# Optimization experiments

Measured on AMD Instinct MI355X. Metric: run time of the kernel, lower is better.

## Reference

```python
import jax, jax.numpy as jnp
import numpy as np

B, T, D = 2, 2048, 1024
H = 16
HD = D // H
SCALE = 1.0 / np.sqrt(HD).astype(np.float32)


def setup_inputs() -> dict:
    key = jax.random.key(0)
    ks = jax.random.split(key, 5)
    std = 1.0 / np.sqrt(D).astype(np.float32)
    x = jax.random.normal(ks[0], (B, T, D), dtype=jnp.float32)
    Wqkvt = jax.random.normal(ks[1], (D, 4 * D), dtype=jnp.float32) * std
    bqkvt = jax.random.normal(ks[2], (4 * D,), dtype=jnp.float32) * 0.02
    Wout = jax.random.normal(ks[3], (D, D), dtype=jnp.float32) * std
    bout = jax.random.normal(ks[4], (D,), dtype=jnp.float32) * 0.02
    return {"x": x, "Wqkvt": Wqkvt, "bqkvt": bqkvt, "Wout": Wout, "bout": bout}


def reference(x, Wqkvt, bqkvt, Wout, bout):
    b, t, d = x.shape
    # fused qkvt projection -> [B,T,4,H,HD]
    qkvt = (x @ Wqkvt + bqkvt).reshape(b, t, 4, H, HD)
    # -> [B,H,T,HD] each
    q, k, v, tt = [jnp.transpose(qkvt[:, :, i], (0, 2, 1, 3)) for i in range(4)]

    # standard dot-product scores [B,H,T,T]
    scores_dot = jnp.einsum('bhqd,bhkd->bhqk', q, k)
    # triplet term: (q*t) against cumsum over keys of (k*v)/sqrt(hd)
    kv = k * v * SCALE
    kv_cum = jnp.cumsum(kv, axis=2)  # causal prefix over key positions
    scores_trip = jnp.einsum('bhqd,bhkd->bhqk', q * tt, kv_cum)

    scores = (scores_dot + scores_trip) * SCALE
    causal = jnp.triu(jnp.ones((t, t), dtype=bool), k=1)
    scores = jnp.where(causal[None, None], -jnp.inf, scores)

    attn = jax.nn.softmax(scores, axis=-1)
    out = jnp.einsum('bhqk,bhkd->bhqd', attn, v)  # [B,H,T,HD]
    out = jnp.transpose(out, (0, 2, 1, 3)).reshape(b, t, d)
    return out @ Wout + bout
```

## Files before the change

kernel.cpp:

```cpp
#include <hip/hip_runtime.h>

#define T_SEQ 2048
#define D_MODEL 1024
#define NH 16
#define HD 64
#define BH_TOT 32
#define M_ROWS 4096
#define NT 32
#define SCALE 0.125f
#define BHT (BH_TOT * T_SEQ)
#define LOG2E 1.44269504f
#define TAU 2.885f

typedef _Float16 h8 __attribute__((ext_vector_type(8)));
typedef _Float16 h4 __attribute__((ext_vector_type(4)));
typedef float f32x4 __attribute__((ext_vector_type(4)));

__device__ __forceinline__ f32x4 mfma_h(h8 a, h8 b, f32x4 c) {
    return __builtin_amdgcn_mfma_f32_16x16x32_f16(a, b, c, 0, 0, 0);
}

__device__ __forceinline__ void gload16(const _Float16* g, _Float16* l) {
    __builtin_amdgcn_global_load_lds(
        (const __attribute__((address_space(1))) unsigned int*)g,
        (__attribute__((address_space(3))) unsigned int*)l, 16, 0, 0);
}

__global__ void k_convert(const float* __restrict__ in, _Float16* __restrict__ out, int n) {
    int i = (blockIdx.x * blockDim.x + threadIdx.x) * 4;
    if (i < n) {
        float4 v = *(const float4*)(in + i);
        h4 o;
        o[0] = (_Float16)v.x; o[1] = (_Float16)v.y;
        o[2] = (_Float16)v.z; o[3] = (_Float16)v.w;
        *(h4*)(out + i) = o;
    }
}

__global__ void k_transpose(const float* __restrict__ in, _Float16* __restrict__ out, int K, int N) {
    __shared__ float tile[32][33];
    int nb = blockIdx.x * 32, kb = blockIdx.y * 32;
    int tx = threadIdx.x & 31, ty = threadIdx.x >> 5;
    #pragma unroll
    for (int i = 0; i < 32; i += 8)
        tile[ty + i][tx] = in[(size_t)(kb + ty + i) * N + (nb + tx)];
    __syncthreads();
    #pragma unroll
    for (int i = 0; i < 32; i += 8)
        out[(size_t)(nb + ty + i) * K + (kb + tx)] = (_Float16)tile[tx][ty + i];
}

template<int MODE>
__launch_bounds__(256, 2)
__global__ void k_gemm(const _Float16* __restrict__ A, const _Float16* __restrict__ Bt,
                       int M, int N, int K, const float* __restrict__ bias,
                       _Float16* __restrict__ qo, _Float16* __restrict__ kho,
                       _Float16* __restrict__ kfo, _Float16* __restrict__ vo,
                       _Float16* __restrict__ vfo, _Float16* __restrict__ to,
                       float* __restrict__ cOut)
{
    __shared__ __align__(16) _Float16 lA[2][128 * 64];
    __shared__ __align__(16) _Float16 lB[2][128 * 64];
    const int tid = threadIdx.x;
    const int wid = tid >> 6, lane = tid & 63, lrow = lane & 15, lg = lane >> 4;
    const int wm = wid >> 1, wn = wid & 1;
    const int m0 = blockIdx.x * 128, n0 = blockIdx.y * 128;

    f32x4 acc[4][4];
    #pragma unroll
    for (int i = 0; i < 4; i++)
        #pragma unroll
        for (int j = 0; j < 4; j++) acc[i][j] = (f32x4){0.f, 0.f, 0.f, 0.f};

    const int rin = lane >> 3, gcol = lane & 7;
    const int scol = (gcol ^ rin) * 8;
    const _Float16* gA = A + (size_t)(m0 + 32 * wid + rin) * K + scol;
    const _Float16* gB = Bt + (size_t)(n0 + 32 * wid + rin) * K + scol;

    const int r7 = lrow & 7;
    const int nk = K >> 6;

    #pragma unroll
    for (int i = 0; i < 4; i++) {
        gload16(gA + (size_t)(8 * i) * K, &lA[0][32 * wid * 64 + 8 * i * 64]);
        gload16(gB + (size_t)(8 * i) * K, &lB[0][32 * wid * 64 + 8 * i * 64]);
    }
    __syncthreads();

    for (int kt = 0; kt < nk; ++kt) {
        const int cur = kt & 1;
        if (kt + 1 < nk) {
            const size_t ko = (size_t)(kt + 1) * 64;
            #pragma unroll
            for (int i = 0; i < 4; i++) {
                gload16(gA + (size_t)(8 * i) * K + ko, &lA[cur ^ 1][32 * wid * 64 + 8 * i * 64]);
                gload16(gB + (size_t)(8 * i) * K + ko, &lB[cur ^ 1][32 * wid * 64 + 8 * i * 64]);
            }
        }
        h8 af[4][2], bfr[4][2];
        #pragma unroll
        for (int mi = 0; mi < 4; mi++) {
            const int row = wm * 64 + mi * 16 + lrow;
            af[mi][0] = *(const h8*)&lA[cur][row * 64 + ((lg ^ r7) * 8)];
            af[mi][1] = *(const h8*)&lA[cur][row * 64 + (((4 + lg) ^ r7) * 8)];
        }
        #pragma unroll
        for (int ni = 0; ni < 4; ni++) {
            const int row = wn * 64 + ni * 16 + lrow;
            bfr[ni][0] = *(const h8*)&lB[cur][row * 64 + ((lg ^ r7) * 8)];
            bfr[ni][1] = *(const h8*)&lB[cur][row * 64 + (((4 + lg) ^ r7) * 8)];
        }
        #pragma unroll
        for (int mi = 0; mi < 4; mi++)
            #pragma unroll
            for (int ni = 0; ni < 4; ni++) {
                acc[mi][ni] = mfma_h(af[mi][0], bfr[ni][0], acc[mi][ni]);
                acc[mi][ni] = mfma_h(af[mi][1], bfr[ni][1], acc[mi][ni]);
            }
        __syncthreads();
    }

    if (MODE == 0) {
        const int ssel = n0 >> 10;
        #pragma unroll
        for (int mi = 0; mi < 4; mi++) {
            #pragma unroll
            for (int ni = 0; ni < 4; ni++) {
                const int nn = n0 + wn * 64 + ni * 16 + lrow;
                const float bv = bias[nn];
                const int h = (nn >> 6) & 15, hd = nn & 63;
                const int mmb = m0 + wm * 64 + mi * 16 + 4 * lg;
                const int b = mmb >> 11, t0 = mmb & (T_SEQ - 1);
                const int bh = b * NH + h;
                const size_t rowb = (size_t)bh * T_SEQ;
                h4 hv;
                #pragma unroll
                for (int r = 0; r < 4; r++) hv[r] = (_Float16)(acc[mi][ni][r] + bv);
                if (ssel == 0) {
                    #pragma unroll
                    for (int r = 0; r < 4; r++) qo[(rowb + t0 + r) * HD + hd] = hv[r];
                } else if (ssel == 1) {
                    const int ksK = hd >> 5, lgK = (hd & 31) >> 3, iK = hd & 7;
                    #pragma unroll
                    for (int r = 0; r < 4; r++) {
                        const int t = t0 + r;
                        kho[(rowb + t) * HD + hd] = hv[r];
                        const int j = t >> 6, ct = (t >> 4) & 3;
                        const int laneF = (t & 15) | (lgK << 4);
                        kfo[(((size_t)bh * 32 + j) * 16 + ct * 4 + ksK) * 512 + laneF * 8 + iK] = hv[r];
                    }
                } else if (ssel == 2) {
                    #pragma unroll
                    for (int r = 0; r < 4; r++) vo[(rowb + t0 + r) * HD + hd] = hv[r];
                    const int ctV = hd >> 4, lrV = hd & 15;
                    const int j = t0 >> 6, ksV = (t0 >> 5) & 1, lgV = (t0 >> 3) & 3, i0 = t0 & 7;
                    const int laneF = lrV | (lgV << 4);
                    *(h4*)&vfo[(((size_t)bh * 32 + j) * 8 + ctV * 2 + ksV) * 512 + laneF * 8 + i0] = hv;
                } else {
                    #pragma unroll
                    for (int r = 0; r < 4; r++) to[(rowb + t0 + r) * HD + hd] = hv[r];
                }
            }
        }
    } else {
        #pragma unroll
        for (int mi = 0; mi < 4; mi++) {
            #pragma unroll
            for (int ni = 0; ni < 4; ni++) {
                const int nn = n0 + wn * 64 + ni * 16 + lrow;
                const float bv = bias[nn];
                #pragma unroll
                for (int r = 0; r < 4; r++) {
                    const int mm = m0 + wm * 64 + mi * 16 + 4 * lg + r;
                    cOut[(size_t)mm * N + nn] = acc[mi][ni][r] + bv;
                }
            }
        }
    }
}

__global__ void k_kvcum(const _Float16* __restrict__ Kh, const _Float16* __restrict__ Vh,
                        _Float16* __restrict__ KF)
{
    const int bh = blockIdx.x;
    const int w = threadIdx.x >> 6, d = threadIdx.x & 63;
    const size_t base = (size_t)bh * T_SEQ * HD + d;
    const int CH = T_SEQ / 16;
    const int t0 = w * CH;
    float s = 0.f;
    for (int i = 0; i < CH; i++) {
        size_t o = base + (size_t)(t0 + i) * HD;
        s += (float)Kh[o] * (float)Vh[o];
    }
    __shared__ float tot[16][64];
    tot[w][d] = s;
    __syncthreads();
    float acc = 0.f;
    for (int ww = 0; ww < w; ww++) acc += tot[ww][d];
    const int ksK = 2 + (d >> 5), lgK = (d & 31) >> 3, iK = d & 7;
    for (int i = 0; i < CH; i++) {
        const int t = t0 + i;
        size_t o = base + (size_t)t * HD;
        acc += (float)Kh[o] * (float)Vh[o];
        const int j = t >> 6, ct = (t >> 4) & 3;
        const int laneF = (t & 15) | (lgK << 4);
        KF[(((size_t)bh * 32 + j) * 16 + ct * 4 + ksK) * 512 + laneF * 8 + iK] =
            (_Float16)(acc * SCALE);
    }
}

__launch_bounds__(256, 4)
__global__ void k_attn(const _Float16* __restrict__ Qb, const _Float16* __restrict__ Tb,
                       const _Float16* __restrict__ KF, const _Float16* __restrict__ VF,
                       _Float16* __restrict__ Op0, _Float16* __restrict__ Op1,
                       _Float16* __restrict__ Op2, _Float16* __restrict__ Op3,
                       float* __restrict__ ML, int nsplit)
{
    const int bh = blockIdx.x;
    const int pair = blockIdx.y;
    const int ksel = blockIdx.z;
    const int tid = threadIdx.x;
    const int wid = tid >> 6, lane = tid & 63, lrow = lane & 15, lg = lane >> 4;
    const _Float16* qp = Qb + (size_t)bh * T_SEQ * HD;
    const _Float16* tp = Tb + (size_t)bh * T_SEQ * HD;
    const _Float16* kfb = KF + (size_t)bh * 32 * 16 * 512;
    const _Float16* vfb = VF + (size_t)bh * 32 * 8 * 512;
    _Float16* op = (ksel == 0) ? Op0 : (ksel == 1) ? Op1 : (ksel == 2) ? Op2 : Op3;
    float* ml = ML + (size_t)ksel * BHT * 2;

    __shared__ __align__(16) _Float16 lP[4][16 * 64];

    const h8 ones = {(_Float16)1.f, (_Float16)1.f, (_Float16)1.f, (_Float16)1.f,
                     (_Float16)1.f, (_Float16)1.f, (_Float16)1.f, (_Float16)1.f};
    const float C = SCALE * LOG2E;

    for (int half = 0; half < 2; ++half) {
        const int qi = half ? (NT - 1 - pair) : pair;
        const int q0 = qi * 64;
        const int nj = qi + 1;
        const int jbeg = (nj * ksel) / nsplit;
        const int jend = (nj * (ksel + 1)) / nsplit;

        const int qrow = q0 + wid * 16 + lrow;
        h8 qf[4];
        #pragma unroll
        for (int ks = 0; ks < 2; ++ks) {
            h8 qv = *(const h8*)&qp[(size_t)qrow * HD + ks * 32 + lg * 8];
            h8 tv = *(const h8*)&tp[(size_t)qrow * HD + ks * 32 + lg * 8];
            h8 a2, b2;
            #pragma unroll
            for (int i = 0; i < 8; i++) {
                float qq = (float)qv[i] * C;
                a2[i] = (_Float16)qq;
                b2[i] = (_Float16)(qq * (float)tv[i]);
            }
            qf[ks] = a2; qf[2 + ks] = b2;
        }

        float m_r[4];
        f32x4 o[4], o4;
        #pragma unroll
        for (int r = 0; r < 4; r++) m_r[r] = -__builtin_inff();
        #pragma unroll
        for (int ct = 0; ct < 4; ct++) o[ct] = (f32x4){0.f, 0.f, 0.f, 0.f};
        o4 = (f32x4){0.f, 0.f, 0.f, 0.f};

        for (int j = jbeg; j < jend; ++j) {
            f32x4 s[4];
            #pragma unroll
            for (int ct = 0; ct < 4; ct++) {
                const _Float16* kb = kfb + ((size_t)j * 16 + ct * 4) * 512 + lane * 8;
                f32x4 sv = (f32x4){0.f, 0.f, 0.f, 0.f};
                sv = mfma_h(qf[0], *(const h8*)kb, sv);
                sv = mfma_h(qf[1], *(const h8*)(kb + 512), sv);
                sv = mfma_h(qf[2], *(const h8*)(kb + 1024), sv);
                sv = mfma_h(qf[3], *(const h8*)(kb + 1536), sv);
                s[ct] = sv;
            }
            if (j == qi) {
                #pragma unroll
                for (int ct = 0; ct < 4; ct++)
                    #pragma unroll
                    for (int r = 0; r < 4; r++) {
                        int key = j * 64 + ct * 16 + lrow;
                        int qr  = q0 + wid * 16 + 4 * lg + r;
                        if (key > qr) s[ct][r] = -__builtin_inff();
                    }
            }
            float mx[4];
            #pragma unroll
            for (int r = 0; r < 4; r++)
                mx[r] = fmaxf(fmaxf(s[0][r], s[1][r]), fmaxf(s[2][r], s[3][r]));
            bool need = (mx[0] > m_r[0] + TAU) | (mx[1] > m_r[1] + TAU) |
                        (mx[2] > m_r[2] + TAU) | (mx[3] > m_r[3] + TAU);
            if (__any(need)) {
                #pragma unroll
                for (int d = 1; d < 16; d <<= 1)
                    #pragma unroll
                    for (int r = 0; r < 4; r++) mx[r] = fmaxf(mx[r], __shfl_xor(mx[r], d, 64));
                #pragma unroll
                for (int r = 0; r < 4; r++) {
                    float mn = fmaxf(m_r[r], mx[r]);
                    float scl = __builtin_amdgcn_exp2f(m_r[r] - mn);
                    o[0][r] *= scl; o[1][r] *= scl; o[2][r] *= scl; o[3][r] *= scl;
                    o4[r] *= scl;
                    m_r[r] = mn;
                }
            }
            #pragma unroll
            for (int ct = 0; ct < 4; ct++) {
                const int col = ct * 16 + lrow;
                #pragma unroll
                for (int r = 0; r < 4; r++) {
                    float p = __builtin_amdgcn_exp2f(s[ct][r] - m_r[r]);
                    const int row = 4 * lg + r;
                    const int boff = row * 128 + ((col * 2) ^ ((row & 7) << 4) ^ ((row & 12) << 3));
                    lP[wid][boff >> 1] = (_Float16)p;
                }
            }
            h8 pa[2];
            #pragma unroll
            for (int ks = 0; ks < 2; ks++) {
                const int boff = lrow * 128 +
                    ((ks * 64 + lg * 16) ^ ((lrow & 7) << 4) ^ ((lrow & 12) << 3));
                pa[ks] = *(const h8*)((const char*)lP[wid] + boff);
            }
            o4 = mfma_h(pa[0], ones, o4);
            o4 = mfma_h(pa[1], ones, o4);
            #pragma unroll
            for (int ct = 0; ct < 4; ct++) {
                const _Float16* vb = vfb + ((size_t)j * 8 + ct * 2) * 512 + lane * 8;
                o[ct] = mfma_h(pa[0], *(const h8*)vb, o[ct]);
                o[ct] = mfma_h(pa[1], *(const h8*)(vb + 512), o[ct]);
            }
        }
        #pragma unroll
        for (int ct = 0; ct < 4; ct++)
            #pragma unroll
            for (int r = 0; r < 4; r++) {
                const int trow = q0 + wid * 16 + 4 * lg + r;
                const int d = ct * 16 + lrow;
                op[((size_t)bh * T_SEQ + trow) * HD + d] = (_Float16)o[ct][r];
            }
        if (lrow == 0) {
            #pragma unroll
            for (int r = 0; r < 4; r++) {
                const int trow = q0 + wid * 16 + 4 * lg + r;
                const size_t mi = ((size_t)bh * T_SEQ + trow) * 2;
                ml[mi] = m_r[r];
                ml[mi + 1] = o4[r];
            }
        }
    }
}

__global__ void k_combine(const _Float16* __restrict__ Op0, const _Float16* __restrict__ Op1,
                          const _Float16* __restrict__ Op2, const _Float16* __restrict__ Op3,
                          const float* __restrict__ ML, _Float16* __restrict__ AO, int nsplit)
{
    const int idx = blockIdx.x * 256 + threadIdx.x;
    const int row = idx >> 3;
    const int d0 = (idx & 7) * 8;
    const int bh = row >> 11, t = row & (T_SEQ - 1);
    const int b = bh >> 4, h = bh & 15;
    const _Float16* ops[4] = {Op0, Op1, Op2, Op3};
    float m = -__builtin_inff();
    for (int c = 0; c < nsplit; c++) m = fmaxf(m, ML[(size_t)c * BHT * 2 + 2 * row]);
    float w[4], denom = 0.f;
    for (int c = 0; c < nsplit; c++) {
        w[c] = __builtin_amdgcn_exp2f(ML[(size_t)c * BHT * 2 + 2 * row] - m);
        denom += w[c] * ML[(size_t)c * BHT * 2 + 2 * row + 1];
    }
    const float inv = 1.0f / denom;
    float accv[8];
    #pragma unroll
    for (int i = 0; i < 8; i++) accv[i] = 0.f;
    for (int c = 0; c < nsplit; c++) {
        h8 a = *(const h8*)&ops[c][(size_t)row * HD + d0];
        #pragma unroll
        for (int i = 0; i < 8; i++) accv[i] += w[c] * (float)a[i];
    }
    h8 r;
    #pragma unroll
    for (int i = 0; i < 8; i++) r[i] = (_Float16)(accv[i] * inv);
    *(h8*)&AO[((size_t)(b * T_SEQ + t)) * D_MODEL + h * HD + d0] = r;
}

extern "C" void kernel_launch(void* const* d_in, const int* in_sizes, int n_in,
                              void* d_out, int out_size, void* d_ws, size_t ws_size,
                              hipStream_t stream)
{
    const float* x     = (const float*)d_in[0];
    const float* Wqkvt = (const float*)d_in[1];
    const float* bqkvt = (const float*)d_in[2];
    const float* Wout  = (const float*)d_in[3];
    const float* bout  = (const float*)d_in[4];
    float* out = (float*)d_out;

    char* ws = (char*)d_ws;
    size_t off = 0;
    auto alloc = [&](size_t bytes) {
        char* p = ws + off;
        off += (bytes + 255) & ~(size_t)255;
        return p;
    };
    const size_t SZ = (size_t)M_ROWS * D_MODEL * 2;
    _Float16* xb  = (_Float16*)alloc(SZ);
    _Float16* wt  = (_Float16*)alloc(SZ);
    _Float16* wo  = (_Float16*)alloc((size_t)D_MODEL * D_MODEL * 2);
    _Float16* Qh  = (_Float16*)alloc(SZ);
    _Float16* Kh  = (_Float16*)alloc(SZ);
    _Float16* Vh  = (_Float16*)alloc(SZ);
    _Float16* Th  = (_Float16*)alloc(SZ);
    _Float16* KF  = (_Float16*)alloc(SZ * 2);
    _Float16* VF  = (_Float16*)alloc(SZ);
    _Float16* AO  = (_Float16*)alloc(SZ);
    _Float16* Op3 = (_Float16*)alloc(SZ);
    const size_t need4 = off;

    const int nsplit = (ws_size >= need4) ? 4 : 2;

    _Float16* Op0 = xb;
    _Float16* Op1 = Vh;
    _Float16* Op2 = Kh;
    float*    ML  = (float*)wt;

    k_convert<<<4096, 256, 0, stream>>>(x, xb, M_ROWS * D_MODEL);
    k_transpose<<<dim3(128, 32), 256, 0, stream>>>(Wqkvt, wt, D_MODEL, 4 * D_MODEL);
    k_transpose<<<dim3(32, 32), 256, 0, stream>>>(Wout, wo, D_MODEL, D_MODEL);
    k_gemm<0><<<dim3(32, 32), 256, 0, stream>>>(xb, wt, M_ROWS, 4 * D_MODEL, D_MODEL,
                                                bqkvt, Qh, Kh, KF, Vh, VF, Th, nullptr);
    k_kvcum<<<BH_TOT, 1024, 0, stream>>>(Kh, Vh, KF);
    k_attn<<<dim3(BH_TOT, NT / 2, nsplit), 256, 0, stream>>>(Qh, Th, KF, VF,
                                                             Op0, Op1, Op2, Op3, ML, nsplit);
    k_combine<<<BHT * HD / 8 / 256, 256, 0, stream>>>(Op0, Op1, Op2, Op3, ML, AO, nsplit);
    k_gemm<1><<<dim3(32, 8), 256, 0, stream>>>(AO, wo, M_ROWS, D_MODEL, D_MODEL,
                                               bout, nullptr, nullptr, nullptr, nullptr,
                                               nullptr, nullptr, out);
}
```

Baseline: 187.5 us.

## Process two 16-row query tiles per wave in attention to reuse K/V fragments

The attention kernel now launches 128 threads (2 waves) per block, and each wave handles 32 query rows as two 16-row sub-tiles instead of one. Each K and V fragment loaded from global memory is reused across both sub-tiles' MFMAs, halving K/V load traffic per query row. The cost is doubled per-wave register state (accumulators, scores, max trackers) under new launch bounds of (128, 2), plus fewer waves per block and less latency hiding.

```diff
diff --git a/kernel.cpp b/kernel.cpp
--- a/kernel.cpp
+++ b/kernel.cpp
@@ -209,7 +209,7 @@
     }
 }
 
-__launch_bounds__(256, 4)
+__launch_bounds__(128, 2)
 __global__ void k_attn(const _Float16* __restrict__ Qb, const _Float16* __restrict__ Tb,
                        const _Float16* __restrict__ KF, const _Float16* __restrict__ VF,
                        _Float16* __restrict__ Op0, _Float16* __restrict__ Op1,
@@ -241,114 +241,155 @@
         const int jbeg = (nj * ksel) / nsplit;
         const int jend = (nj * (ksel + 1)) / nsplit;
 
-        const int qrow = q0 + wid * 16 + lrow;
-        h8 qf[4];
-        #pragma unroll
-        for (int ks = 0; ks < 2; ++ks) {
-            h8 qv = *(const h8*)&qp[(size_t)qrow * HD + ks * 32 + lg * 8];
-            h8 tv = *(const h8*)&tp[(size_t)qrow * HD + ks * 32 + lg * 8];
-            h8 a2, b2;
-            #pragma unroll
-            for (int i = 0; i < 8; i++) {
-                float qq = (float)qv[i] * C;
-                a2[i] = (_Float16)qq;
-                b2[i] = (_Float16)(qq * (float)tv[i]);
-            }
-            qf[ks] = a2; qf[2 + ks] = b2;
-        }
-
-        float m_r[4];
-        f32x4 o[4], o4;
-        #pragma unroll
-        for (int r = 0; r < 4; r++) m_r[r] = -__builtin_inff();
-        #pragma unroll
-        for (int ct = 0; ct < 4; ct++) o[ct] = (f32x4){0.f, 0.f, 0.f, 0.f};
-        o4 = (f32x4){0.f, 0.f, 0.f, 0.f};
+        h8 qf[2][4];
+        #pragma unroll
+        for (int u = 0; u < 2; ++u) {
+            const int qrow = q0 + wid * 32 + u * 16 + lrow;
+            #pragma unroll
+            for (int ks = 0; ks < 2; ++ks) {
+                h8 qv = *(const h8*)&qp[(size_t)qrow * HD + ks * 32 + lg * 8];
+                h8 tv = *(const h8*)&tp[(size_t)qrow * HD + ks * 32 + lg * 8];
+                h8 a2, b2;
+                #pragma unroll
+                for (int i = 0; i < 8; i++) {
+                    float qq = (float)qv[i] * C;
+                    a2[i] = (_Float16)qq;
+                    b2[i] = (_Float16)(qq * (float)tv[i]);
+                }
+                qf[u][ks] = a2; qf[u][2 + ks] = b2;
+            }
+        }
+
+        float m_r[2][4];
+        f32x4 o[2][4], o4[2];
+        #pragma unroll
+        for (int u = 0; u < 2; u++) {
+            #pragma unroll
+            for (int r = 0; r < 4; r++) m_r[u][r] = -__builtin_inff();
+            #pragma unroll
+            for (int ct = 0; ct < 4; ct++) o[u][ct] = (f32x4){0.f, 0.f, 0.f, 0.f};
+            o4[u] = (f32x4){0.f, 0.f, 0.f, 0.f};
+        }
 
         for (int j = jbeg; j < jend; ++j) {
-            f32x4 s[4];
+            f32x4 s[2][4];
             #pragma unroll
             for (int ct = 0; ct < 4; ct++) {
                 const _Float16* kb = kfb + ((size_t)j * 16 + ct * 4) * 512 + lane * 8;
-                f32x4 sv = (f32x4){0.f, 0.f, 0.f, 0.f};
-                sv = mfma_h(qf[0], *(const h8*)kb, sv);
-                sv = mfma_h(qf[1], *(const h8*)(kb + 512), sv);
-                sv = mfma_h(qf[2], *(const h8*)(kb + 1024), sv);
-                sv = mfma_h(qf[3], *(const h8*)(kb + 1536), sv);
-                s[ct] = sv;
+                const h8 k0 = *(const h8*)kb;
+                const h8 k1 = *(const h8*)(kb + 512);
+                const h8 k2 = *(const h8*)(kb + 1024);
+                const h8 k3 = *(const h8*)(kb + 1536);
+                #pragma unroll
+                for (int u = 0; u < 2; u++) {
+                    f32x4 sv = (f32x4){0.f, 0.f, 0.f, 0.f};
+                    sv = mfma_h(qf[u][0], k0, sv);
+                    sv = mfma_h(qf[u][1], k1, sv);
+                    sv = mfma_h(qf[u][2], k2, sv);
+                    sv = mfma_h(qf[u][3], k3, sv);
+                    s[u][ct] = sv;
+                }
             }
             if (j == qi) {
                 #pragma unroll
-                for (int ct = 0; ct < 4; ct++)
+                for (int u = 0; u < 2; u++)
+                    #pragma unroll
+                    for (int ct = 0; ct < 4; ct++)
+                        #pragma unroll
+                        for (int r = 0; r < 4; r++) {
+                            int key = j * 64 + ct * 16 + lrow;
+                            int qr  = q0 + wid * 32 + u * 16 + 4 * lg + r;
+                            if (key > qr) s[u][ct][r] = -__builtin_inff();
+                        }
+            }
+            float mx[2][4];
+            bool need = false;
+            #pragma unroll
+            for (int u = 0; u < 2; u++)
+                #pragma unroll
+                for (int r = 0; r < 4; r++) {
+                    mx[u][r] = fmaxf(fmaxf(s[u][0][r], s[u][1][r]),
+                                     fmaxf(s[u][2][r], s[u][3][r]));
+                    need |= (mx[u][r] > m_r[u][r] + TAU);
+                }
+            if (__any(need)) {
+                #pragma unroll
+                for (int d = 1; d < 16; d <<= 1)
+                    #pragma unroll
+                    for (int u = 0; u < 2; u++)
+                        #pragma unroll
+                        for (int r = 0; r < 4; r++)
+                            mx[u][r] = fmaxf(mx[u][r], __shfl_xor(mx[u][r], d, 64));
+                #pragma unroll
+                for (int u = 0; u < 2; u++)
                     #pragma unroll
                     for (int r = 0; r < 4; r++) {
-                        int key = j * 64 + ct * 16 + lrow;
-                        int qr  = q0 + wid * 16 + 4 * lg + r;
-                        if (key > qr) s[ct][r] = -__builtin_inff();
+                        float mn = fmaxf(m_r[u][r], mx[u][r]);
+                        float scl = __builtin_amdgcn_exp2f(m_r[u][r] - mn);
+                        o[u][0][r] *= scl; o[u][1][r] *= scl;
+                        o[u][2][r] *= scl; o[u][3][r] *= scl;
+                        o4[u][r] *= scl;
+                        m_r[u][r] = mn;
                     }
             }
-            float mx[4];
-            #pragma unroll
-            for (int r = 0; r < 4; r++)
-                mx[r] = fmaxf(fmaxf(s[0][r], s[1][r]), fmaxf(s[2][r], s[3][r]));
-            bool need = (mx[0] > m_r[0] + TAU) | (mx[1] > m_r[1] + TAU) |
-                        (mx[2] > m_r[2] + TAU) | (mx[3] > m_r[3] + TAU);
-            if (__any(need)) {
-                #pragma unroll
-                for (int d = 1; d < 16; d <<= 1)
-                    #pragma unroll
-                    for (int r = 0; r < 4; r++) mx[r] = fmaxf(mx[r], __shfl_xor(mx[r], d, 64));
-                #pragma unroll
-                for (int r = 0; r < 4; r++) {
-                    float mn = fmaxf(m_r[r], mx[r]);
-                    float scl = __builtin_amdgcn_exp2f(m_r[r] - mn);
-                    o[0][r] *= scl; o[1][r] *= scl; o[2][r] *= scl; o[3][r] *= scl;
-                    o4[r] *= scl;
-                    m_r[r] = mn;
-                }
-            }
-            #pragma unroll
-            for (int ct = 0; ct < 4; ct++) {
-                const int col = ct * 16 + lrow;
-                #pragma unroll
-                for (int r = 0; r < 4; r++) {
-                    float p = __builtin_amdgcn_exp2f(s[ct][r] - m_r[r]);
-                    const int row = 4 * lg + r;
-                    const int boff = row * 128 + ((col * 2) ^ ((row & 7) << 4) ^ ((row & 12) << 3));
-                    lP[wid][boff >> 1] = (_Float16)p;
-                }
-            }
-            h8 pa[2];
-            #pragma unroll
-            for (int ks = 0; ks < 2; ks++) {
-                const int boff = lrow * 128 +
-                    ((ks * 64 + lg * 16) ^ ((lrow & 7) << 4) ^ ((lrow & 12) << 3));
-                pa[ks] = *(const h8*)((const char*)lP[wid] + boff);
-            }
-            o4 = mfma_h(pa[0], ones, o4);
-            o4 = mfma_h(pa[1], ones, o4);
+            #pragma unroll
+            for (int u = 0; u < 2; u++)
+                #pragma unroll
+                for (int ct = 0; ct < 4; ct++) {
+                    const int col = ct * 16 + lrow;
+                    #pragma unroll
+                    for (int r = 0; r < 4; r++) {
+                        float p = __builtin_amdgcn_exp2f(s[u][ct][r] - m_r[u][r]);
+                        const int row = 4 * lg + r;
+                        const int boff = row * 128 +
+                            ((col * 2) ^ ((row & 7) << 4) ^ ((row & 12) << 3));
+                        lP[wid * 2 + u][boff >> 1] = (_Float16)p;
+                    }
+                }
+            h8 pa[2][2];
+            #pragma unroll
+            for (int u = 0; u < 2; u++)
+                #pragma unroll
+                for (int ks = 0; ks < 2; ks++) {
+                    const int boff = lrow * 128 +
+                        ((ks * 64 + lg * 16) ^ ((lrow & 7) << 4) ^ ((lrow & 12) << 3));
+                    pa[u][ks] = *(const h8*)((const char*)lP[wid * 2 + u] + boff);
+                }
+            #pragma unroll
+            for (int u = 0; u < 2; u++) {
+                o4[u] = mfma_h(pa[u][0], ones, o4[u]);
+                o4[u] = mfma_h(pa[u][1], ones, o4[u]);
+            }
             #pragma unroll
             for (int ct = 0; ct < 4; ct++) {
                 const _Float16* vb = vfb + ((size_t)j * 8 + ct * 2) * 512 + lane * 8;
-                o[ct] = mfma_h(pa[0], *(const h8*)vb, o[ct]);
-                o[ct] = mfma_h(pa[1], *(const h8*)(vb + 512), o[ct]);
-            }
-        }
-        #pragma unroll
-        for (int ct = 0; ct < 4; ct++)
-            #pragma unroll
-            for (int r = 0; r < 4; r++) {
-                const int trow = q0 + wid * 16 + 4 * lg + r;
-                const int d = ct * 16 + lrow;
-                op[((size_t)bh * T_SEQ + trow) * HD + d] = (_Float16)o[ct][r];
-            }
-        if (lrow == 0) {
-            #pragma unroll
-            for (int r = 0; r < 4; r++) {
-                const int trow = q0 + wid * 16 + 4 * lg + r;
-                const size_t mi = ((size_t)bh * T_SEQ + trow) * 2;
-                ml[mi] = m_r[r];
-                ml[mi + 1] = o4[r];
+                const h8 v0 = *(const h8*)vb;
+                const h8 v1 = *(const h8*)(vb + 512);
+                #pragma unroll
+                for (int u = 0; u < 2; u++) {
+                    o[u][ct] = mfma_h(pa[u][0], v0, o[u][ct]);
+                    o[u][ct] = mfma_h(pa[u][1], v1, o[u][ct]);
+                }
+            }
+        }
+        #pragma unroll
+        for (int u = 0; u < 2; u++) {
+            #pragma unroll
+            for (int ct = 0; ct < 4; ct++)
+                #pragma unroll
+                for (int r = 0; r < 4; r++) {
+                    const int trow = q0 + wid * 32 + u * 16 + 4 * lg + r;
+                    const int d = ct * 16 + lrow;
+                    op[((size_t)bh * T_SEQ + trow) * HD + d] = (_Float16)o[u][ct][r];
+                }
+            if (lrow == 0) {
+                #pragma unroll
+                for (int r = 0; r < 4; r++) {
+                    const int trow = q0 + wid * 32 + u * 16 + 4 * lg + r;
+                    const size_t mi = ((size_t)bh * T_SEQ + trow) * 2;
+                    ml[mi] = m_r[u][r];
+                    ml[mi + 1] = o4[u][r];
+                }
             }
         }
     }
@@ -431,7 +472,7 @@
     k_gemm<0><<<dim3(32, 32), 256, 0, stream>>>(xb, wt, M_ROWS, 4 * D_MODEL, D_MODEL,
                                                 bqkvt, Qh, Kh, KF, Vh, VF, Th, nullptr);
     k_kvcum<<<BH_TOT, 1024, 0, stream>>>(Kh, Vh, KF);
-    k_attn<<<dim3(BH_TOT, NT / 2, nsplit), 256, 0, stream>>>(Qh, Th, KF, VF,
+    k_attn<<<dim3(BH_TOT, NT / 2, nsplit), 128, 0, stream>>>(Qh, Th, KF, VF,
                                                              Op0, Op1, Op2, Op3, ML, nsplit);
     k_combine<<<BHT * HD / 8 / 256, 256, 0, stream>>>(Op0, Op1, Op2, Op3, ML, AO, nsplit);
     k_gemm<1><<<dim3(32, 8), 256, 0, stream>>>(AO, wo, M_ROWS, D_MODEL, D_MODEL,
```

Measured after the change: 191.1 us. No clear change (+1.9%).

## Single-buffer GEMM LDS to raise occupancy and add unroll pragmas

Applied to the files above, without the earlier changes.

The GEMM drops its double-buffered LDS tiles for a single buffer, removing the prefetch of the next K tile and loading each tile synchronously before compute. This halves LDS use, and the launch bounds are raised to allow three blocks per CU so more resident waves can hide global-load latency instead of software pipelining doing it. Unroll pragmas are also added to the kv prefix-sum reduction loop and the attention key-block loop. The trade is losing the overlap of loads with MFMA inside a block, and the tighter launch bound may push up register pressure or cause spills.

```diff
diff --git a/kernel.cpp b/kernel.cpp
--- a/kernel.cpp
+++ b/kernel.cpp
@@ -51,7 +51,7 @@
 }
 
 template<int MODE>
-__launch_bounds__(256, 2)
+__launch_bounds__(256, 3)
 __global__ void k_gemm(const _Float16* __restrict__ A, const _Float16* __restrict__ Bt,
                        int M, int N, int K, const float* __restrict__ bias,
                        _Float16* __restrict__ qo, _Float16* __restrict__ kho,
@@ -59,8 +59,8 @@
                        _Float16* __restrict__ vfo, _Float16* __restrict__ to,
                        float* __restrict__ cOut)
 {
-    __shared__ __align__(16) _Float16 lA[2][128 * 64];
-    __shared__ __align__(16) _Float16 lB[2][128 * 64];
+    __shared__ __align__(16) _Float16 lA[128 * 64];
+    __shared__ __align__(16) _Float16 lB[128 * 64];
     const int tid = threadIdx.x;
     const int wid = tid >> 6, lane = tid & 63, lrow = lane & 15, lg = lane >> 4;
     const int wm = wid >> 1, wn = wid & 1;
@@ -76,39 +76,32 @@
     const int scol = (gcol ^ rin) * 8;
     const _Float16* gA = A + (size_t)(m0 + 32 * wid + rin) * K + scol;
     const _Float16* gB = Bt + (size_t)(n0 + 32 * wid + rin) * K + scol;
+    _Float16* lAw = &lA[32 * wid * 64];
+    _Float16* lBw = &lB[32 * wid * 64];
 
     const int r7 = lrow & 7;
     const int nk = K >> 6;
-
-    #pragma unroll
-    for (int i = 0; i < 4; i++) {
-        gload16(gA + (size_t)(8 * i) * K, &lA[0][32 * wid * 64 + 8 * i * 64]);
-        gload16(gB + (size_t)(8 * i) * K, &lB[0][32 * wid * 64 + 8 * i * 64]);
-    }
-    __syncthreads();
-
     for (int kt = 0; kt < nk; ++kt) {
-        const int cur = kt & 1;
-        if (kt + 1 < nk) {
-            const size_t ko = (size_t)(kt + 1) * 64;
-            #pragma unroll
-            for (int i = 0; i < 4; i++) {
-                gload16(gA + (size_t)(8 * i) * K + ko, &lA[cur ^ 1][32 * wid * 64 + 8 * i * 64]);
-                gload16(gB + (size_t)(8 * i) * K + ko, &lB[cur ^ 1][32 * wid * 64 + 8 * i * 64]);
-            }
-        }
+        const size_t ko = (size_t)kt * 64;
+        #pragma unroll
+        for (int i = 0; i < 4; i++) {
+            gload16(gA + (size_t)(8 * i) * K + ko, lAw + 8 * i * 64);
+            gload16(gB + (size_t)(8 * i) * K + ko, lBw + 8 * i * 64);
+        }
+        __syncthreads();
+
         h8 af[4][2], bfr[4][2];
         #pragma unroll
         for (int mi = 0; mi < 4; mi++) {
             const int row = wm * 64 + mi * 16 + lrow;
-            af[mi][0] = *(const h8*)&lA[cur][row * 64 + ((lg ^ r7) * 8)];
-            af[mi][1] = *(const h8*)&lA[cur][row * 64 + (((4 + lg) ^ r7) * 8)];
+            af[mi][0] = *(const h8*)&lA[row * 64 + ((lg ^ r7) * 8)];
+            af[mi][1] = *(const h8*)&lA[row * 64 + (((4 + lg) ^ r7) * 8)];
         }
         #pragma unroll
         for (int ni = 0; ni < 4; ni++) {
             const int row = wn * 64 + ni * 16 + lrow;
-            bfr[ni][0] = *(const h8*)&lB[cur][row * 64 + ((lg ^ r7) * 8)];
-            bfr[ni][1] = *(const h8*)&lB[cur][row * 64 + (((4 + lg) ^ r7) * 8)];
+            bfr[ni][0] = *(const h8*)&lB[row * 64 + ((lg ^ r7) * 8)];
+            bfr[ni][1] = *(const h8*)&lB[row * 64 + (((4 + lg) ^ r7) * 8)];
         }
         #pragma unroll
         for (int mi = 0; mi < 4; mi++)
@@ -188,6 +181,7 @@
     const int CH = T_SEQ / 16;
     const int t0 = w * CH;
     float s = 0.f;
+    #pragma unroll 8
     for (int i = 0; i < CH; i++) {
         size_t o = base + (size_t)(t0 + i) * HD;
         s += (float)Kh[o] * (float)Vh[o];
@@ -265,6 +259,7 @@
         for (int ct = 0; ct < 4; ct++) o[ct] = (f32x4){0.f, 0.f, 0.f, 0.f};
         o4 = (f32x4){0.f, 0.f, 0.f, 0.f};
 
+        #pragma unroll 2
         for (int j = jbeg; j < jend; ++j) {
             f32x4 s[4];
             #pragma unroll
```

Result: slower. 191.8 us (+2.3%).
